# Performance work log

Hardware: AMD Instinct MI355X
Metric: run time of the kernel (lower is better)

Reference implementation:

```python
import jax, jax.numpy as jnp
import numpy as np

K = 2  # top-k slots from init kwargs


def setup_inputs() -> dict:
    key = jax.random.key(0)
    ks = jax.random.split(key, 6)
    B, T, d, E, dff = 2, 2048, 512, 8, 2048
    x = jax.random.normal(ks[0], (B, T, d), dtype=jnp.float32)
    Wg = jax.random.normal(ks[1], (d, E), dtype=jnp.float32) * 0.02
    W1 = jax.random.normal(ks[2], (E, d, dff), dtype=jnp.float32) * 0.02
    b1 = jnp.zeros((E, dff), dtype=jnp.float32)
    W2 = jax.random.normal(ks[3], (E, dff, d), dtype=jnp.float32) * 0.02
    b2 = jnp.zeros((E, d), dtype=jnp.float32)
    return {"x": x, "Wg": Wg, "W1": W1, "b1": b1, "W2": W2, "b2": b2}


def reference(x, Wg, W1, b1, W2, b2):
    # Gate: softmax over experts, top-k probs renormalized. Note: in the
    # original code the per-expert gather/scatter masks partition the tokens,
    # so dispatched_input == x * p_i (full weighted input), and ALL experts'
    # MLPs are applied to it and summed (tf.add_n). We reproduce that math.
    logits = jnp.einsum('btd,de->bte', x, Wg)          # [B,T,E]
    probs = jax.nn.softmax(logits, axis=-1)
    top_p, _top_i = jax.lax.top_k(probs, K)            # [B,T,K]
    top_p = top_p / jnp.sum(top_p, axis=-1, keepdims=True)
    b2_sum = jnp.sum(b2, axis=0)                        # sum of all experts' output biases
    out = jnp.zeros_like(x)
    for i in range(K):  # small fixed loop over top-k slots
        w_in = x * top_p[..., i:i + 1]                  # [B,T,d]
        # every expert runs on the full weighted input (faithful to source)
        h = jax.nn.gelu(
            jnp.einsum('btd,edf->ebtf', w_in, W1) + b1[:, None, None, :],
            approximate=False)                           # [E,B,T,dff]
        out = out + jnp.einsum('ebtf,efd->btd', h, W2) + b2_sum
    return out
```

## Files before the change

kernel.cpp:

```cpp
#include <hip/hip_runtime.h>
#include <hip/hip_bf16.h>
#include <cstdint>

#define TOKENS 4096
#define DMODEL 512
#define NEXP 8
#define DFF 2048

typedef short s16x8 __attribute__((ext_vector_type(8)));
typedef short s16x4 __attribute__((ext_vector_type(4)));
typedef float f32x4 __attribute__((ext_vector_type(4)));

__device__ __forceinline__ float bf2f(short h) {
    unsigned int u = ((unsigned int)(unsigned short)h) << 16;
    return __uint_as_float(u);
}
__device__ __forceinline__ short f2bf(float f) {
    unsigned int u = __float_as_uint(f);
    u += 0x7fffu + ((u >> 16) & 1u);
    return (short)(u >> 16);
}
__device__ __forceinline__ unsigned int cvtpk_bf16(float a, float b) {
    unsigned int r;
    asm volatile("v_cvt_pk_bf16_f32 %0, %1, %2" : "=v"(r) : "v"(a), "v"(b));
    return r;
}
__device__ __forceinline__ float gelu_sig(float x) {
    float z = x * -2.4554443f;
    float ex = __builtin_amdgcn_exp2f(z);
    float r = __builtin_amdgcn_rcpf(1.0f + ex);
    return x * r;
}
__device__ __forceinline__ float gelu_f(float x) {
    float x2 = x * x;
    float z2 = x * fmaf(x2, 0.07135481627260025f, 1.5957691216057308f);
    float ex = __expf(z2);
    float r = __builtin_amdgcn_rcpf(1.0f + ex);
    return x - x * r;
}
__device__ __forceinline__ void gload_lds16(const void* g, void* l) {
    __builtin_amdgcn_global_load_lds((const __attribute__((address_space(1))) void*)g,
                                     (__attribute__((address_space(3))) void*)l, 16, 0, 0);
}

__global__ void gate_kernel(const float* __restrict__ x, const float* __restrict__ Wg,
                            float* __restrict__ s0, float* __restrict__ s1) {
    int wave = threadIdx.x >> 6;
    int lane = threadIdx.x & 63;
    int t = blockIdx.x * 4 + wave;
    const float* xr = x + (size_t)t * DMODEL + lane * 8;
    float4 xa = *(const float4*)(xr);
    float4 xb = *(const float4*)(xr + 4);
    float xv[8] = {xa.x, xa.y, xa.z, xa.w, xb.x, xb.y, xb.z, xb.w};
    float lg[8];
#pragma unroll
    for (int e = 0; e < 8; e++) lg[e] = 0.f;
#pragma unroll
    for (int j = 0; j < 8; j++) {
        const float4* wr = (const float4*)(Wg + (size_t)(lane * 8 + j) * NEXP);
        float4 wa = wr[0], wb = wr[1];
        lg[0] = fmaf(xv[j], wa.x, lg[0]);
        lg[1] = fmaf(xv[j], wa.y, lg[1]);
        lg[2] = fmaf(xv[j], wa.z, lg[2]);
        lg[3] = fmaf(xv[j], wa.w, lg[3]);
        lg[4] = fmaf(xv[j], wb.x, lg[4]);
        lg[5] = fmaf(xv[j], wb.y, lg[5]);
        lg[6] = fmaf(xv[j], wb.z, lg[6]);
        lg[7] = fmaf(xv[j], wb.w, lg[7]);
    }
#pragma unroll
    for (int off = 32; off > 0; off >>= 1) {
#pragma unroll
        for (int e = 0; e < 8; e++) lg[e] += __shfl_xor(lg[e], off, 64);
    }
    float l0 = lg[0]; int i0 = 0;
#pragma unroll
    for (int e = 1; e < 8; e++) { if (lg[e] > l0) { l0 = lg[e]; i0 = e; } }
    float l1 = -3.4e38f;
#pragma unroll
    for (int e = 0; e < 8; e++) { if (e != i0 && lg[e] > l1) l1 = lg[e]; }
    float p1 = expf(l1 - l0);
    float sa = 1.0f / (1.0f + p1);
    if (lane == 0) { s0[t] = sa; s1[t] = p1 * sa; }
}

__global__ void cvt_x_kernel(const float* __restrict__ x, short* __restrict__ xb) {
    int i = blockIdx.x * blockDim.x + threadIdx.x;
    const float4* p = (const float4*)(x + (size_t)i * 8);
    float4 a = p[0], b = p[1];
    s16x8 v;
    v[0] = f2bf(a.x); v[1] = f2bf(a.y); v[2] = f2bf(a.z); v[3] = f2bf(a.w);
    v[4] = f2bf(b.x); v[5] = f2bf(b.y); v[6] = f2bf(b.z); v[7] = f2bf(b.w);
    *(s16x8*)(xb + (size_t)i * 8) = v;
}

__global__ void transpose_cvt_kernel(const float* __restrict__ in, short* __restrict__ out,
                                     int R, int C) {
    __shared__ float t[64][33];
    int b = blockIdx.z;
    const float* ip = in + (size_t)b * R * C;
    short* op = out + (size_t)b * R * C;
    int c0 = blockIdx.x * 64, r0 = blockIdx.y * 32;
    int tid = threadIdx.x;
    int lr = tid >> 3, lc8 = (tid & 7) * 8;
    const float* src = &ip[(size_t)(r0 + lr) * C + c0 + lc8];
    float4 v0 = *(const float4*)src;
    float4 v1 = *(const float4*)(src + 4);
    t[lc8 + 0][lr] = v0.x; t[lc8 + 1][lr] = v0.y; t[lc8 + 2][lr] = v0.z; t[lc8 + 3][lr] = v0.w;
    t[lc8 + 4][lr] = v1.x; t[lc8 + 5][lr] = v1.y; t[lc8 + 6][lr] = v1.z; t[lc8 + 7][lr] = v1.w;
    __syncthreads();
    int sc = tid >> 2, sk = (tid & 3) * 8;
    s16x8 o;
#pragma unroll
    for (int j = 0; j < 8; j++) o[j] = f2bf(t[sc][sk + j]);
    *(s16x8*)&op[(size_t)(c0 + sc) * R + r0 + sk] = o;
}

__launch_bounds__(256, 2)
__global__ void gemm1_kernel(const short* __restrict__ xb, const short* __restrict__ w1t,
                             short* __restrict__ Y) {
    __shared__ short Al[128 * 64];
    __shared__ short Bl[128 * 64];
    int d = blockIdx.x;
    int e = d & 7;
    int tno = d >> 3;
    int n0 = (tno & 15) * 128;
    int m0 = (tno >> 4) * 128;
    const short* A = xb;
    const short* B = w1t + (size_t)e * DFF * DMODEL;
    short* Yo = Y + (size_t)e * TOKENS * DFF;

    int tid = threadIdx.x;
    int lane = tid & 63;
    int w = tid >> 6;
    int m_off = (w >> 1) * 64;
    int n_off = (w & 1) * 64;

    int srow = lane >> 3;
    int schunk = (lane & 7) ^ srow;
    int q = lane >> 4;

    f32x4 acc[4][4];
#pragma unroll
    for (int mi = 0; mi < 4; mi++)
#pragma unroll
        for (int ni = 0; ni < 4; ni++) acc[mi][ni] = (f32x4){0.f, 0.f, 0.f, 0.f};

    for (int k0 = 0; k0 < DMODEL; k0 += 64) {
#pragma unroll
        for (int c = 0; c < 4; c++) {
            int seg = c * 4 + w;
            gload_lds16(&A[(size_t)(m0 + seg * 8 + srow) * DMODEL + k0 + schunk * 8],
                        &Al[seg * 512]);
            gload_lds16(&B[(size_t)(n0 + seg * 8 + srow) * DMODEL + k0 + schunk * 8],
                        &Bl[seg * 512]);
        }
        __syncthreads();
#pragma unroll
        for (int ks = 0; ks < 2; ks++) {
            s16x8 af[4], bfr[4];
#pragma unroll
            for (int mi = 0; mi < 4; mi++) {
                int r = m_off + mi * 16 + (lane & 15);
                int cp = (ks * 4 + q) ^ (r & 7);
                af[mi] = *(const s16x8*)&Al[r * 64 + cp * 8];
            }
#pragma unroll
            for (int ni = 0; ni < 4; ni++) {
                int r = n_off + ni * 16 + (lane & 15);
                int cp = (ks * 4 + q) ^ (r & 7);
                bfr[ni] = *(const s16x8*)&Bl[r * 64 + cp * 8];
            }
#pragma unroll
            for (int mi = 0; mi < 4; mi++)
#pragma unroll
                for (int ni = 0; ni < 4; ni++)
                    acc[mi][ni] = __builtin_amdgcn_mfma_f32_16x16x32_bf16(af[mi], bfr[ni], acc[mi][ni], 0, 0, 0);
        }
        __syncthreads();
    }
#pragma unroll
    for (int mi = 0; mi < 4; mi++)
#pragma unroll
        for (int ni = 0; ni < 4; ni++) {
            int row = m0 + m_off + mi * 16 + (lane >> 4) * 4;
            int col = n0 + n_off + ni * 16 + (lane & 15);
#pragma unroll
            for (int r = 0; r < 4; r++)
                Yo[(size_t)(row + r) * DFF + col] = f2bf(acc[mi][ni][r]);
        }
}

__launch_bounds__(512, 4)
__global__ void gemm2_kernel(const short* __restrict__ Y, const short* __restrict__ w2t,
                             const float* __restrict__ s0v, const float* __restrict__ s1v,
                             const float* __restrict__ b1, float* __restrict__ part) {
    __shared__ short Bl[512 * 32];
    __shared__ short Hs[64 * 32];
    int d = blockIdx.x;
    int e = d & 7;
    int m0 = (d >> 3) * 64;
    const short* Ye = Y + (size_t)e * TOKENS * DFF;
    const short* B = w2t + (size_t)e * DMODEL * DFF;
    const float* b1e = b1 + (size_t)e * DFF;
    float* Pe = part + (size_t)e * TOKENS * DMODEL;

    int tid = threadIdx.x;
    int lane = tid & 63;
    int w = tid >> 6;
    int n_off = w * 64;
    int q = lane >> 4;

    int hrow = tid >> 3;
    int off8 = tid & 7;
    int hcol = off8 * 4;
    int hchunk16 = off8 >> 1, hsub = off8 & 1;
    int hcp = hchunk16 ^ ((hrow >> 1) & 3);
    unsigned int* hdst = (unsigned int*)((char*)Hs + hrow * 64 + hcp * 16 + hsub * 8);
    float sa = s0v[m0 + hrow], sb = s1v[m0 + hrow];

    int brow = lane >> 2;
    int bsrc = (lane & 3) ^ ((lane >> 3) & 3);

    f32x4 acc[4][4];
#pragma unroll
    for (int mi = 0; mi < 4; mi++)
#pragma unroll
        for (int ni = 0; ni < 4; ni++) acc[mi][ni] = (f32x4){0.f, 0.f, 0.f, 0.f};

    for (int f0 = 0; f0 < DFF; f0 += 32) {
#pragma unroll
        for (int c = 0; c < 4; c++) {
            int seg = c * 8 + w;
            gload_lds16(&B[(size_t)(seg * 16 + brow) * DFF + f0 + bsrc * 8],
                        &Bl[seg * 512]);
        }
        {
            s16x4 yv = *(const s16x4*)&Ye[(size_t)(m0 + hrow) * DFF + f0 + hcol];
            float4 bb = *(const float4*)&b1e[f0 + hcol];
            float bbv[4] = {bb.x, bb.y, bb.z, bb.w};
            float hs[4];
#pragma unroll
            for (int j = 0; j < 4; j++) {
                float yf = bf2f(yv[j]);
                float h0 = fmaf(sa, yf, bbv[j]);
                float h1 = fmaf(sb, yf, bbv[j]);
                hs[j] = gelu_sig(h0) + gelu_sig(h1);
            }
            hdst[0] = cvtpk_bf16(hs[0], hs[1]);
            hdst[1] = cvtpk_bf16(hs[2], hs[3]);
        }
        __syncthreads();
        {
            s16x8 af[4];
#pragma unroll
            for (int mi = 0; mi < 4; mi++) {
                int r = mi * 16 + (lane & 15);
                int cp = q ^ ((r >> 1) & 3);
                af[mi] = *(const s16x8*)&Hs[r * 32 + cp * 8];
            }
#pragma unroll
            for (int ni = 0; ni < 4; ni++) {
                int r = n_off + ni * 16 + (lane & 15);
                int cp = q ^ ((r >> 1) & 3);
                s16x8 bfr = *(const s16x8*)&Bl[r * 32 + cp * 8];
#pragma unroll
                for (int mi = 0; mi < 4; mi++)
                    acc[mi][ni] = __builtin_amdgcn_mfma_f32_16x16x32_bf16(af[mi], bfr, acc[mi][ni], 0, 0, 0);
            }
        }
        __syncthreads();
    }
#pragma unroll
    for (int mi = 0; mi < 4; mi++)
#pragma unroll
        for (int ni = 0; ni < 4; ni++) {
            int row = m0 + mi * 16 + (lane >> 4) * 4;
            int col = n_off + ni * 16 + (lane & 15);
#pragma unroll
            for (int r = 0; r < 4; r++)
                Pe[(size_t)(row + r) * DMODEL + col] = acc[mi][ni][r];
        }
}

__global__ void reduce_kernel(const float* __restrict__ part, const float* __restrict__ b2,
                              float* __restrict__ out) {
    int i = (blockIdx.x * 256 + threadIdx.x) * 4;
    if (i >= TOKENS * DMODEL) return;
    int n = i & (DMODEL - 1);
    float4 s = {0.f, 0.f, 0.f, 0.f};
    float4 bs = {0.f, 0.f, 0.f, 0.f};
#pragma unroll
    for (int e = 0; e < 8; e++) {
        float4 p = *(const float4*)&part[(size_t)e * TOKENS * DMODEL + i];
        s.x += p.x; s.y += p.y; s.z += p.z; s.w += p.w;
        float4 b = *(const float4*)&b2[(size_t)e * DMODEL + n];
        bs.x += b.x; bs.y += b.y; bs.z += b.z; bs.w += b.w;
    }
    s.x += 2.f * bs.x; s.y += 2.f * bs.y; s.z += 2.f * bs.z; s.w += 2.f * bs.w;
    *(float4*)&out[i] = s;
}

extern "C" void kernel_launch(void* const* d_in, const int* in_sizes, int n_in,
                              void* d_out, int out_size, void* d_ws, size_t ws_size,
                              hipStream_t stream) {
    const float* x  = (const float*)d_in[0];
    const float* Wg = (const float*)d_in[1];
    const float* W1 = (const float*)d_in[2];
    const float* b1 = (const float*)d_in[3];
    const float* W2 = (const float*)d_in[4];
    const float* b2 = (const float*)d_in[5];
    float* out = (float*)d_out;

    char* ws = (char*)d_ws;
    float* s0  = (float*)(ws);
    float* s1  = (float*)(ws + 16384);
    short* xb  = (short*)(ws + 32768);
    short* w1t = (short*)(ws + 32768 + 4194304);
    short* w2t = (short*)(ws + 32768 + 4194304 + 16777216);
    short* Yb  = (short*)(ws + 32768 + 4194304 + 2ull * 16777216);
    float* part= (float*)(ws + 32768 + 4194304 + 2ull * 16777216 + 134217728);

    hipLaunchKernelGGL(gate_kernel, dim3(1024), dim3(256), 0, stream, x, Wg, s0, s1);
    hipLaunchKernelGGL(cvt_x_kernel, dim3(1024), dim3(256), 0, stream, x, xb);
    hipLaunchKernelGGL(transpose_cvt_kernel, dim3(32, 16, 8), dim3(256), 0, stream, W1, w1t, 512, 2048);
    hipLaunchKernelGGL(transpose_cvt_kernel, dim3(8, 64, 8), dim3(256), 0, stream, W2, w2t, 2048, 512);
    hipLaunchKernelGGL(gemm1_kernel, dim3(4096), dim3(256), 0, stream, xb, w1t, Yb);
    hipLaunchKernelGGL(gemm2_kernel, dim3(512), dim3(512), 0, stream, Yb, w2t, s0, s1, b1, part);
    hipLaunchKernelGGL(reduce_kernel, dim3(2048), dim3(256), 0, stream, part, b2, out);
}
```

Before: 235.3 us.

## Double-buffer gemm2 LDS tiles, fuse gate with x conversion, use tanh-form GELU

```diff
diff --git a/kernel.cpp b/kernel.cpp
--- a/kernel.cpp
+++ b/kernel.cpp
@@ -24,12 +24,6 @@
     unsigned int r;
     asm volatile("v_cvt_pk_bf16_f32 %0, %1, %2" : "=v"(r) : "v"(a), "v"(b));
     return r;
-}
-__device__ __forceinline__ float gelu_sig(float x) {
-    float z = x * -2.4554443f;
-    float ex = __builtin_amdgcn_exp2f(z);
-    float r = __builtin_amdgcn_rcpf(1.0f + ex);
-    return x * r;
 }
 __device__ __forceinline__ float gelu_f(float x) {
     float x2 = x * x;
@@ -43,15 +37,21 @@
                                      (__attribute__((address_space(3))) void*)l, 16, 0, 0);
 }
 
-__global__ void gate_kernel(const float* __restrict__ x, const float* __restrict__ Wg,
-                            float* __restrict__ s0, float* __restrict__ s1) {
+__global__ void gate_cvt_kernel(const float* __restrict__ x, const float* __restrict__ Wg,
+                                float* __restrict__ s0, float* __restrict__ s1,
+                                short* __restrict__ xb) {
     int wave = threadIdx.x >> 6;
     int lane = threadIdx.x & 63;
     int t = blockIdx.x * 4 + wave;
     const float* xr = x + (size_t)t * DMODEL + lane * 8;
     float4 xa = *(const float4*)(xr);
-    float4 xb = *(const float4*)(xr + 4);
-    float xv[8] = {xa.x, xa.y, xa.z, xa.w, xb.x, xb.y, xb.z, xb.w};
+    float4 xv2 = *(const float4*)(xr + 4);
+    float xv[8] = {xa.x, xa.y, xa.z, xa.w, xv2.x, xv2.y, xv2.z, xv2.w};
+    s16x8 v;
+#pragma unroll
+    for (int j = 0; j < 8; j++) v[j] = f2bf(xv[j]);
+    *(s16x8*)&xb[(size_t)t * DMODEL + lane * 8] = v;
+
     float lg[8];
 #pragma unroll
     for (int e = 0; e < 8; e++) lg[e] = 0.f;
@@ -82,16 +82,6 @@
     float p1 = expf(l1 - l0);
     float sa = 1.0f / (1.0f + p1);
     if (lane == 0) { s0[t] = sa; s1[t] = p1 * sa; }
-}
-
-__global__ void cvt_x_kernel(const float* __restrict__ x, short* __restrict__ xb) {
-    int i = blockIdx.x * blockDim.x + threadIdx.x;
-    const float4* p = (const float4*)(x + (size_t)i * 8);
-    float4 a = p[0], b = p[1];
-    s16x8 v;
-    v[0] = f2bf(a.x); v[1] = f2bf(a.y); v[2] = f2bf(a.z); v[3] = f2bf(a.w);
-    v[4] = f2bf(b.x); v[5] = f2bf(b.y); v[6] = f2bf(b.z); v[7] = f2bf(b.w);
-    *(s16x8*)(xb + (size_t)i * 8) = v;
 }
 
 __global__ void transpose_cvt_kernel(const float* __restrict__ in, short* __restrict__ out,
@@ -195,8 +185,8 @@
 __global__ void gemm2_kernel(const short* __restrict__ Y, const short* __restrict__ w2t,
                              const float* __restrict__ s0v, const float* __restrict__ s1v,
                              const float* __restrict__ b1, float* __restrict__ part) {
-    __shared__ short Bl[512 * 32];
-    __shared__ short Hs[64 * 32];
+    __shared__ short Bl[2][512 * 32];
+    __shared__ short Hs[2][64 * 32];
     int d = blockIdx.x;
     int e = d & 7;
     int m0 = (d >> 3) * 64;
@@ -216,8 +206,9 @@
     int hcol = off8 * 4;
     int hchunk16 = off8 >> 1, hsub = off8 & 1;
     int hcp = hchunk16 ^ ((hrow >> 1) & 3);
-    unsigned int* hdst = (unsigned int*)((char*)Hs + hrow * 64 + hcp * 16 + hsub * 8);
+    int hoff_bytes = hrow * 64 + hcp * 16 + hsub * 8;
     float sa = s0v[m0 + hrow], sb = s1v[m0 + hrow];
+    const short* yrow = &Ye[(size_t)(m0 + hrow) * DFF + hcol];
 
     int brow = lane >> 2;
     int bsrc = (lane & 3) ^ ((lane >> 3) & 3);
@@ -228,49 +219,79 @@
 #pragma unroll
         for (int ni = 0; ni < 4; ni++) acc[mi][ni] = (f32x4){0.f, 0.f, 0.f, 0.f};
 
-    for (int f0 = 0; f0 < DFF; f0 += 32) {
-#pragma unroll
-        for (int c = 0; c < 4; c++) {
-            int seg = c * 8 + w;
-            gload_lds16(&B[(size_t)(seg * 16 + brow) * DFF + f0 + bsrc * 8],
-                        &Bl[seg * 512]);
-        }
-        {
-            s16x4 yv = *(const s16x4*)&Ye[(size_t)(m0 + hrow) * DFF + f0 + hcol];
-            float4 bb = *(const float4*)&b1e[f0 + hcol];
-            float bbv[4] = {bb.x, bb.y, bb.z, bb.w};
-            float hs[4];
-#pragma unroll
-            for (int j = 0; j < 4; j++) {
-                float yf = bf2f(yv[j]);
-                float h0 = fmaf(sa, yf, bbv[j]);
-                float h1 = fmaf(sb, yf, bbv[j]);
-                hs[j] = gelu_sig(h0) + gelu_sig(h1);
-            }
-            hdst[0] = cvtpk_bf16(hs[0], hs[1]);
-            hdst[1] = cvtpk_bf16(hs[2], hs[3]);
-        }
-        __syncthreads();
+#pragma unroll
+    for (int c = 0; c < 4; c++) {
+        int seg = c * 8 + w;
+        gload_lds16(&B[(size_t)(seg * 16 + brow) * DFF + bsrc * 8], &Bl[0][seg * 512]);
+    }
+    {
+        s16x4 yv = *(const s16x4*)yrow;
+        float4 bb = *(const float4*)&b1e[hcol];
+        float bbv[4] = {bb.x, bb.y, bb.z, bb.w};
+        float hs4[4];
+#pragma unroll
+        for (int j = 0; j < 4; j++) {
+            float yf = bf2f(yv[j]);
+            hs4[j] = gelu_f(fmaf(sa, yf, bbv[j])) + gelu_f(fmaf(sb, yf, bbv[j]));
+        }
+        unsigned int* hd = (unsigned int*)((char*)&Hs[0][0] + hoff_bytes);
+        hd[0] = cvtpk_bf16(hs4[0], hs4[1]);
+        hd[1] = cvtpk_bf16(hs4[2], hs4[3]);
+    }
+    __syncthreads();
+
+    const int NT = DFF / 32;
+    for (int f = 0; f < NT; f++) {
+        int cur = f & 1;
+        const short* Blc = &Bl[cur][0];
+        const short* Hsc = &Hs[cur][0];
+        s16x4 yn;
+        float4 bn;
+        bool more = (f + 1 < NT);
+        if (more) {
+            int f1 = (f + 1) * 32;
+#pragma unroll
+            for (int c = 0; c < 4; c++) {
+                int seg = c * 8 + w;
+                gload_lds16(&B[(size_t)(seg * 16 + brow) * DFF + f1 + bsrc * 8],
+                            &Bl[cur ^ 1][seg * 512]);
+            }
+            yn = *(const s16x4*)(yrow + f1);
+            bn = *(const float4*)&b1e[f1 + hcol];
+        }
         {
             s16x8 af[4];
 #pragma unroll
             for (int mi = 0; mi < 4; mi++) {
                 int r = mi * 16 + (lane & 15);
                 int cp = q ^ ((r >> 1) & 3);
-                af[mi] = *(const s16x8*)&Hs[r * 32 + cp * 8];
+                af[mi] = *(const s16x8*)&Hsc[r * 32 + cp * 8];
             }
 #pragma unroll
             for (int ni = 0; ni < 4; ni++) {
                 int r = n_off + ni * 16 + (lane & 15);
                 int cp = q ^ ((r >> 1) & 3);
-                s16x8 bfr = *(const s16x8*)&Bl[r * 32 + cp * 8];
+                s16x8 bfr = *(const s16x8*)&Blc[r * 32 + cp * 8];
 #pragma unroll
                 for (int mi = 0; mi < 4; mi++)
                     acc[mi][ni] = __builtin_amdgcn_mfma_f32_16x16x32_bf16(af[mi], bfr, acc[mi][ni], 0, 0, 0);
             }
         }
+        if (more) {
+            float bbv[4] = {bn.x, bn.y, bn.z, bn.w};
+            float hs4[4];
+#pragma unroll
+            for (int j = 0; j < 4; j++) {
+                float yf = bf2f(yn[j]);
+                hs4[j] = gelu_f(fmaf(sa, yf, bbv[j])) + gelu_f(fmaf(sb, yf, bbv[j]));
+            }
+            unsigned int* hd = (unsigned int*)((char*)&Hs[cur ^ 1][0] + hoff_bytes);
+            hd[0] = cvtpk_bf16(hs4[0], hs4[1]);
+            hd[1] = cvtpk_bf16(hs4[2], hs4[3]);
+        }
         __syncthreads();
     }
+
 #pragma unroll
     for (int mi = 0; mi < 4; mi++)
 #pragma unroll
@@ -321,8 +342,7 @@
     short* Yb  = (short*)(ws + 32768 + 4194304 + 2ull * 16777216);
     float* part= (float*)(ws + 32768 + 4194304 + 2ull * 16777216 + 134217728);
 
-    hipLaunchKernelGGL(gate_kernel, dim3(1024), dim3(256), 0, stream, x, Wg, s0, s1);
-    hipLaunchKernelGGL(cvt_x_kernel, dim3(1024), dim3(256), 0, stream, x, xb);
+    hipLaunchKernelGGL(gate_cvt_kernel, dim3(1024), dim3(256), 0, stream, x, Wg, s0, s1, xb);
     hipLaunchKernelGGL(transpose_cvt_kernel, dim3(32, 16, 8), dim3(256), 0, stream, W1, w1t, 512, 2048);
     hipLaunchKernelGGL(transpose_cvt_kernel, dim3(8, 64, 8), dim3(256), 0, stream, W2, w2t, 2048, 512);
     hipLaunchKernelGGL(gemm1_kernel, dim3(4096), dim3(256), 0, stream, xb, w1t, Yb);
```

Measured after the change: 244.3 us. 3.8% more time.

## Move GELU epilogue into gemm1, fuse x conversion into gate kernel

Applied to the files above, without the earlier changes.

```diff
diff --git a/kernel.cpp b/kernel.cpp
--- a/kernel.cpp
+++ b/kernel.cpp
@@ -19,17 +19,6 @@
     unsigned int u = __float_as_uint(f);
     u += 0x7fffu + ((u >> 16) & 1u);
     return (short)(u >> 16);
-}
-__device__ __forceinline__ unsigned int cvtpk_bf16(float a, float b) {
-    unsigned int r;
-    asm volatile("v_cvt_pk_bf16_f32 %0, %1, %2" : "=v"(r) : "v"(a), "v"(b));
-    return r;
-}
-__device__ __forceinline__ float gelu_sig(float x) {
-    float z = x * -2.4554443f;
-    float ex = __builtin_amdgcn_exp2f(z);
-    float r = __builtin_amdgcn_rcpf(1.0f + ex);
-    return x * r;
 }
 __device__ __forceinline__ float gelu_f(float x) {
     float x2 = x * x;
@@ -43,15 +32,21 @@
                                      (__attribute__((address_space(3))) void*)l, 16, 0, 0);
 }
 
-__global__ void gate_kernel(const float* __restrict__ x, const float* __restrict__ Wg,
-                            float* __restrict__ s0, float* __restrict__ s1) {
+__global__ void gate_cvt_kernel(const float* __restrict__ x, const float* __restrict__ Wg,
+                                float* __restrict__ s0, float* __restrict__ s1,
+                                short* __restrict__ xb) {
     int wave = threadIdx.x >> 6;
     int lane = threadIdx.x & 63;
     int t = blockIdx.x * 4 + wave;
     const float* xr = x + (size_t)t * DMODEL + lane * 8;
     float4 xa = *(const float4*)(xr);
-    float4 xb = *(const float4*)(xr + 4);
-    float xv[8] = {xa.x, xa.y, xa.z, xa.w, xb.x, xb.y, xb.z, xb.w};
+    float4 xv2 = *(const float4*)(xr + 4);
+    float xv[8] = {xa.x, xa.y, xa.z, xa.w, xv2.x, xv2.y, xv2.z, xv2.w};
+    s16x8 v;
+#pragma unroll
+    for (int j = 0; j < 8; j++) v[j] = f2bf(xv[j]);
+    *(s16x8*)&xb[(size_t)t * DMODEL + lane * 8] = v;
+
     float lg[8];
 #pragma unroll
     for (int e = 0; e < 8; e++) lg[e] = 0.f;
@@ -82,16 +77,6 @@
     float p1 = expf(l1 - l0);
     float sa = 1.0f / (1.0f + p1);
     if (lane == 0) { s0[t] = sa; s1[t] = p1 * sa; }
-}
-
-__global__ void cvt_x_kernel(const float* __restrict__ x, short* __restrict__ xb) {
-    int i = blockIdx.x * blockDim.x + threadIdx.x;
-    const float4* p = (const float4*)(x + (size_t)i * 8);
-    float4 a = p[0], b = p[1];
-    s16x8 v;
-    v[0] = f2bf(a.x); v[1] = f2bf(a.y); v[2] = f2bf(a.z); v[3] = f2bf(a.w);
-    v[4] = f2bf(b.x); v[5] = f2bf(b.y); v[6] = f2bf(b.z); v[7] = f2bf(b.w);
-    *(s16x8*)(xb + (size_t)i * 8) = v;
 }
 
 __global__ void transpose_cvt_kernel(const float* __restrict__ in, short* __restrict__ out,
@@ -118,9 +103,11 @@
 
 __launch_bounds__(256, 2)
 __global__ void gemm1_kernel(const short* __restrict__ xb, const short* __restrict__ w1t,
-                             short* __restrict__ Y) {
+                             const float* __restrict__ s0v, const float* __restrict__ s1v,
+                             const float* __restrict__ b1, short* __restrict__ H) {
     __shared__ short Al[128 * 64];
     __shared__ short Bl[128 * 64];
+    __shared__ float ls0[128], ls1[128], lb1[128];
     int d = blockIdx.x;
     int e = d & 7;
     int tno = d >> 3;
@@ -128,13 +115,19 @@
     int m0 = (tno >> 4) * 128;
     const short* A = xb;
     const short* B = w1t + (size_t)e * DFF * DMODEL;
-    short* Yo = Y + (size_t)e * TOKENS * DFF;
+    short* Ho = H + (size_t)e * TOKENS * DFF;
 
     int tid = threadIdx.x;
     int lane = tid & 63;
     int w = tid >> 6;
     int m_off = (w >> 1) * 64;
     int n_off = (w & 1) * 64;
+
+    if (tid < 128) {
+        ls0[tid] = s0v[m0 + tid];
+        ls1[tid] = s1v[m0 + tid];
+        lb1[tid] = b1[(size_t)e * DFF + n0 + tid];
+    }
 
     int srow = lane >> 3;
     int schunk = (lane & 7) ^ srow;
@@ -180,29 +173,35 @@
         __syncthreads();
     }
 #pragma unroll
-    for (int mi = 0; mi < 4; mi++)
+    for (int mi = 0; mi < 4; mi++) {
+        int rl = m_off + mi * 16 + (lane >> 4) * 4;
+        float sa4[4], sb4[4];
+#pragma unroll
+        for (int r = 0; r < 4; r++) { sa4[r] = ls0[rl + r]; sb4[r] = ls1[rl + r]; }
 #pragma unroll
         for (int ni = 0; ni < 4; ni++) {
-            int row = m0 + m_off + mi * 16 + (lane >> 4) * 4;
-            int col = n0 + n_off + ni * 16 + (lane & 15);
-#pragma unroll
-            for (int r = 0; r < 4; r++)
-                Yo[(size_t)(row + r) * DFF + col] = f2bf(acc[mi][ni][r]);
-        }
+            int cl = n_off + ni * 16 + (lane & 15);
+            float bb = lb1[cl];
+#pragma unroll
+            for (int r = 0; r < 4; r++) {
+                float a = acc[mi][ni][r];
+                float h = gelu_f(fmaf(sa4[r], a, bb)) + gelu_f(fmaf(sb4[r], a, bb));
+                Ho[(size_t)(m0 + rl + r) * DFF + n0 + cl] = f2bf(h);
+            }
+        }
+    }
 }
 
 __launch_bounds__(512, 4)
-__global__ void gemm2_kernel(const short* __restrict__ Y, const short* __restrict__ w2t,
-                             const float* __restrict__ s0v, const float* __restrict__ s1v,
-                             const float* __restrict__ b1, float* __restrict__ part) {
+__global__ void gemm2_kernel(const short* __restrict__ H, const short* __restrict__ w2t,
+                             float* __restrict__ part) {
+    __shared__ short Al[64 * 32];
     __shared__ short Bl[512 * 32];
-    __shared__ short Hs[64 * 32];
     int d = blockIdx.x;
     int e = d & 7;
     int m0 = (d >> 3) * 64;
-    const short* Ye = Y + (size_t)e * TOKENS * DFF;
+    const short* A = H + (size_t)e * TOKENS * DFF;
     const short* B = w2t + (size_t)e * DMODEL * DFF;
-    const float* b1e = b1 + (size_t)e * DFF;
     float* Pe = part + (size_t)e * TOKENS * DMODEL;
 
     int tid = threadIdx.x;
@@ -211,16 +210,8 @@
     int n_off = w * 64;
     int q = lane >> 4;
 
-    int hrow = tid >> 3;
-    int off8 = tid & 7;
-    int hcol = off8 * 4;
-    int hchunk16 = off8 >> 1, hsub = off8 & 1;
-    int hcp = hchunk16 ^ ((hrow >> 1) & 3);
-    unsigned int* hdst = (unsigned int*)((char*)Hs + hrow * 64 + hcp * 16 + hsub * 8);
-    float sa = s0v[m0 + hrow], sb = s1v[m0 + hrow];
-
-    int brow = lane >> 2;
-    int bsrc = (lane & 3) ^ ((lane >> 3) & 3);
+    int srow = lane >> 2;
+    int schunk = (lane & 3) ^ ((lane >> 3) & 3);
 
     f32x4 acc[4][4];
 #pragma unroll
@@ -232,23 +223,12 @@
 #pragma unroll
         for (int c = 0; c < 4; c++) {
             int seg = c * 8 + w;
-            gload_lds16(&B[(size_t)(seg * 16 + brow) * DFF + f0 + bsrc * 8],
+            gload_lds16(&B[(size_t)(seg * 16 + srow) * DFF + f0 + schunk * 8],
                         &Bl[seg * 512]);
         }
-        {
-            s16x4 yv = *(const s16x4*)&Ye[(size_t)(m0 + hrow) * DFF + f0 + hcol];
-            float4 bb = *(const float4*)&b1e[f0 + hcol];
-            float bbv[4] = {bb.x, bb.y, bb.z, bb.w};
-            float hs[4];
-#pragma unroll
-            for (int j = 0; j < 4; j++) {
-                float yf = bf2f(yv[j]);
-                float h0 = fmaf(sa, yf, bbv[j]);
-                float h1 = fmaf(sb, yf, bbv[j]);
-                hs[j] = gelu_sig(h0) + gelu_sig(h1);
-            }
-            hdst[0] = cvtpk_bf16(hs[0], hs[1]);
-            hdst[1] = cvtpk_bf16(hs[2], hs[3]);
+        if (w < 4) {
+            gload_lds16(&A[(size_t)(m0 + w * 16 + srow) * DFF + f0 + schunk * 8],
+                        &Al[w * 512]);
         }
         __syncthreads();
         {
@@ -257,7 +237,7 @@
             for (int mi = 0; mi < 4; mi++) {
                 int r = mi * 16 + (lane & 15);
                 int cp = q ^ ((r >> 1) & 3);
-                af[mi] = *(const s16x8*)&Hs[r * 32 + cp * 8];
+                af[mi] = *(const s16x8*)&Al[r * 32 + cp * 8];
             }
 #pragma unroll
             for (int ni = 0; ni < 4; ni++) {
@@ -271,6 +251,7 @@
         }
         __syncthreads();
     }
+
 #pragma unroll
     for (int mi = 0; mi < 4; mi++)
 #pragma unroll
@@ -318,14 +299,13 @@
     short* xb  = (short*)(ws + 32768);
     short* w1t = (short*)(ws + 32768 + 4194304);
     short* w2t = (short*)(ws + 32768 + 4194304 + 16777216);
-    short* Yb  = (short*)(ws + 32768 + 4194304 + 2ull * 16777216);
+    short* Hb  = (short*)(ws + 32768 + 4194304 + 2ull * 16777216);
     float* part= (float*)(ws + 32768 + 4194304 + 2ull * 16777216 + 134217728);
 
-    hipLaunchKernelGGL(gate_kernel, dim3(1024), dim3(256), 0, stream, x, Wg, s0, s1);
-    hipLaunchKernelGGL(cvt_x_kernel, dim3(1024), dim3(256), 0, stream, x, xb);
+    hipLaunchKernelGGL(gate_cvt_kernel, dim3(1024), dim3(256), 0, stream, x, Wg, s0, s1, xb);
     hipLaunchKernelGGL(transpose_cvt_kernel, dim3(32, 16, 8), dim3(256), 0, stream, W1, w1t, 512, 2048);
     hipLaunchKernelGGL(transpose_cvt_kernel, dim3(8, 64, 8), dim3(256), 0, stream, W2, w2t, 2048, 512);
-    hipLaunchKernelGGL(gemm1_kernel, dim3(4096), dim3(256), 0, stream, xb, w1t, Yb);
-    hipLaunchKernelGGL(gemm2_kernel, dim3(512), dim3(512), 0, stream, Yb, w2t, s0, s1, b1, part);
+    hipLaunchKernelGGL(gemm1_kernel, dim3(4096), dim3(256), 0, stream, xb, w1t, s0, s1, b1, Hb);
+    hipLaunchKernelGGL(gemm2_kernel, dim3(512), dim3(512), 0, stream, Hb, w2t, part);
     hipLaunchKernelGGL(reduce_kernel, dim3(2048), dim3(256), 0, stream, part, b2, out);
 }
```

Result: no change. 238.4 us (+1.3%).
